# Optimization experiments

Measured on AMD Instinct MI355X. Metric: run time of the kernel, lower is better.

The kernel has to match this reference:

```python
import jax, jax.numpy as jnp
import numpy as np

B, S, T, E, H = 16, 96, 50, 128, 128
D2 = 2 * H
V = 32000
NGRAM = 2
ALPHA = 0.25


def _lstm(x, Wih, Whh, b, reverse=False):
    # x: [N, T, E] -> outputs [N, T, H], final h, c (PyTorch gate order i,f,g,o)
    xt = jnp.swapaxes(x, 0, 1)
    if reverse:
        xt = xt[::-1]
    n = x.shape[0]
    h = Whh.shape[1]
    init = (jnp.zeros((n, h), x.dtype), jnp.zeros((n, h), x.dtype))

    def step(carry, xin):
        hprev, cprev = carry
        g = xin @ Wih.T + hprev @ Whh.T + b
        i, f, gg, o = jnp.split(g, 4, axis=-1)
        c = jax.nn.sigmoid(f) * cprev + jax.nn.sigmoid(i) * jnp.tanh(gg)
        hnew = jax.nn.sigmoid(o) * jnp.tanh(c)
        return (hnew, c), hnew

    (hT, cT), outs = jax.lax.scan(step, init, xt)
    if reverse:
        outs = outs[::-1]
    return jnp.swapaxes(outs, 0, 1), hT, cT


def _gru(x, h, Wi, Wh, bi, bh):
    # PyTorch GRUCell, gate order r,z,n
    gi = x @ Wi.T + bi
    gh = h @ Wh.T + bh
    ir, iz, inn = jnp.split(gi, 3, axis=-1)
    hr, hz, hn = jnp.split(gh, 3, axis=-1)
    r = jax.nn.sigmoid(ir + hr)
    z = jax.nn.sigmoid(iz + hz)
    n = jnp.tanh(inn + r * hn)
    return (1.0 - z) * n + z * h


def _norm_scale(x):
    # (||x|| + alpha) / (||x|| + 1), detached as in the original
    v = jnp.linalg.norm(x, axis=1)
    return jax.lax.stop_gradient(((v + ALPHA) / (v + 1.0))[:, None])


def setup_inputs() -> dict:
    key = jax.random.key(0)
    ks = jax.random.split(key, 30)
    rn = lambda k, sh: jax.random.normal(k, sh, jnp.float32) * 0.05
    return {
        "enc_batch": jax.random.randint(ks[0], (B * S, T), 0, V),
        "struct_parent": jax.random.randint(ks[1], (B, S, S), 0, B * S + 1),
        "struct_child": jax.random.randint(ks[2], (B, S, S), 0, B * S + 1),
        "mask_emb": (jax.random.uniform(ks[3], (B, S, S, 1)) < 0.2).astype(jnp.float32),
        "emb_table": rn(ks[4], (V, E)),
        "Wih_f": rn(ks[5], (4 * H, E)), "Whh_f": rn(ks[6], (4 * H, H)), "b_f": rn(ks[7], (4 * H,)),
        "Wih_b": rn(ks[8], (4 * H, E)), "Whh_b": rn(ks[9], (4 * H, H)), "b_b": rn(ks[10], (4 * H,)),
        "Wc": rn(ks[11], (H, D2)), "bc": rn(ks[12], (H,)),
        "Whr": rn(ks[13], (H, D2)), "bhr": rn(ks[14], (H,)),
        "Wi_cp": rn(ks[15], (3 * D2, D2)), "Wh_cp": rn(ks[16], (3 * D2, D2)),
        "bi_cp": rn(ks[17], (3 * D2,)), "bh_cp": rn(ks[18], (3 * D2,)),
        "Wi_pc": rn(ks[19], (3 * D2, D2)), "Wh_pc": rn(ks[20], (3 * D2, D2)),
        "bi_pc": rn(ks[21], (3 * D2,)), "bh_pc": rn(ks[22], (3 * D2,)),
    }


def reference(enc_batch, struct_parent, struct_child, mask_emb, emb_table,
              Wih_f, Whh_f, b_f, Wih_b, Whh_b, b_b, Wc, bc, Whr, bhr,
              Wi_cp, Wh_cp, bi_cp, bh_cp, Wi_pc, Wh_pc, bi_pc, bh_pc):
    # Sentence encoder (bidirectional LSTM); dropout=0 -> identity
    emb = emb_table[enc_batch]                       # [B*S, T, E]
    _, hf, cf = _lstm(emb, Wih_f, Whh_f, b_f)
    _, hb, cb = _lstm(emb, Wih_b, Whh_b, b_b, reverse=True)
    c_red = jax.nn.relu(jnp.concatenate([cf, cb], 1) @ Wc.T + bc)
    h_red = jax.nn.relu(jnp.concatenate([hf, hb], 1) @ Whr.T + bhr)
    enc_states = jnp.concatenate([c_red, h_red], 1)  # [B*S, 2H]
    zero = jnp.zeros((1, D2), enc_states.dtype)
    hidden = jnp.concatenate([zero, enc_states], 0)  # [B*S+1, 2H]; row 0 = zero_emb

    # child -> parent message passing
    for _ in range(NGRAM):
        p = hidden[struct_parent].reshape(-1, D2)    # gather [B*S*S, 2H]
        c = hidden[struct_child].reshape(-1, D2)
        ch = _gru(c, p, Wi_cp, Wh_cp, bi_cp, bh_cp).reshape(B, S, S, D2)
        ch = (ch * mask_emb).sum(1).reshape(B * S, D2)
        ch = jnp.concatenate([zero, ch], 0)
        hidden = hidden + ch * _norm_scale(ch)

    # parent -> child message passing
    for _ in range(NGRAM):
        p = hidden[struct_parent].reshape(-1, D2)
        c = hidden[struct_child].reshape(-1, D2)
        ch = _gru(p, c, Wi_pc, Wh_pc, bi_pc, bh_pc).reshape(B, S, S, D2)
        ch = (ch * mask_emb).sum(2).reshape(B * S, D2)
        ch = jnp.concatenate([zero, ch], 0)
        hidden = hidden + ch * _norm_scale(ch)

    return hidden
```

## Files before the change

kernel.cpp:

```cpp
#include <hip/hip_runtime.h>

typedef unsigned short u16;
typedef __attribute__((ext_vector_type(8))) short bf8;
typedef __attribute__((ext_vector_type(4))) short s16x4;
typedef __attribute__((ext_vector_type(4))) float f32x4;
typedef __attribute__((ext_vector_type(4))) int   i32x4;
typedef __attribute__((ext_vector_type(2))) int   i32x2;

#define S_   96
#define T_   50
#define NSEQ 1536
#define NR   1537
#define XROW 520
#define L2E   1.4426950408889634f
#define L2E2  2.8853900817779268f

__device__ __forceinline__ float bf2f(u16 u){ return __uint_as_float(((unsigned)u)<<16); }
__device__ __forceinline__ u16 f2bf(float f){
  unsigned u = __float_as_uint(f);
  u += 0x7fffu + ((u>>16)&1u);
  return (u16)(u>>16);
}
__device__ __forceinline__ int cvtpk(float lo, float hi){
  int r; asm("v_cvt_pk_bf16_f32 %0, %1, %2" : "=v"(r) : "v"(lo), "v"(hi)); return r;
}
#if __has_builtin(__builtin_amdgcn_exp2f)
__device__ __forceinline__ float exp2_(float x){ return __builtin_amdgcn_exp2f(x); }
#else
__device__ __forceinline__ float exp2_(float x){ return exp2f(x); }
#endif
__device__ __forceinline__ float sigm(float x){
  return __builtin_amdgcn_rcpf(1.f + __expf(-x));
}
__device__ __forceinline__ float tanh_(float x){
  return 1.f - 2.f*__builtin_amdgcn_rcpf(__expf(2.f*x) + 1.f);
}
__device__ __forceinline__ void bar_lds(){
  asm volatile("s_waitcnt lgkmcnt(0)\n\ts_barrier" ::: "memory");
}

struct CvtArgs { const float* s[10]; u16* d[10]; };
__global__ __launch_bounds__(256) void prep_kernel(CvtArgs a,
    const int* __restrict__ par, const int* __restrict__ chi,
    const float* __restrict__ mask,
    int2* __restrict__ ent0, int* __restrict__ cnt0,
    int2* __restrict__ ent1, int* __restrict__ cnt1)
{
  if (blockIdx.x < 1088){
    int e = (blockIdx.x*256 + threadIdx.x)*4;
    if (e >= 1114112) return;
    int t, off;
    if (e < 262144){ t = e>>16; off = e & 65535; }
    else if (e < 327680){ int e2=e-262144; t = 4+(e2>>15); off = e2&32767; }
    else { int e3=e-327680; t = 6 + e3/196608; off = e3%196608; }
    int src = off;
    if (t < 4){
      int colp = off>>7, k = off&127;
      int orig = ((colp>>4)&3)*128 + ((colp>>6)<<4) + (colp&15);
      src = orig*128 + k;
    }
    f32x4 v = *reinterpret_cast<const f32x4*>(a.s[t]+src);
    i32x2 o;
    o[0] = cvtpk(v[0], v[1]);
    o[1] = cvtpk(v[2], v[3]);
    *reinterpret_cast<i32x2*>(a.d[t]+off) = o;
  } else {
    const int rr = blockIdx.x - 1088;
    __shared__ int c0s, c1s;
    if (threadIdx.x==0){ c0s=0; c1s=0; }
    __syncthreads();
    const int l = threadIdx.x;
    if (l < S_){
      const int b = rr/S_, fx = rr%S_, base = b*S_*S_;
      int idx = base + l*S_ + fx;
      if (mask[idx] != 0.f){
        int p = atomicAdd(&c0s, 1);
        ent0[rr*S_ + p] = make_int2(chi[idx], par[idx]);
      }
      int jdx = base + fx*S_ + l;
      if (mask[jdx] != 0.f){
        int p = atomicAdd(&c1s, 1);
        ent1[rr*S_ + p] = make_int2(par[jdx], chi[jdx]);
      }
    }
    __syncthreads();
    if (threadIdx.x==0){ cnt0[rr]=c0s; cnt1[rr]=c1s; }
  }
}

__global__ __launch_bounds__(512, 2) void lstm_kernel(
    const int* __restrict__ enc, const float* __restrict__ emb,
    const u16* __restrict__ WihF, const u16* __restrict__ WhhF, const float* __restrict__ bF,
    const u16* __restrict__ WihB, const u16* __restrict__ WhhB, const float* __restrict__ bB,
    u16* __restrict__ c_cat, u16* __restrict__ h_cat)
{
  __shared__ short xh[16*XROW];
  __shared__ int   toks[16*T_];

  const int tid  = threadIdx.x;
  const int wave = tid>>6;
  const int lane = tid&63;
  const int dir  = blockIdx.y;
  const int s0   = blockIdx.x*16;

  const u16* Wih = dir ? WihB : WihF;
  const u16* Whh = dir ? WhhB : WhhF;
  const float* bb = dir ? bB  : bF;

  for (int i=tid; i<16*T_; i+=512)
    toks[i] = enc[(s0 + i/T_)*T_ + (i%T_)];

  const int mL   = lane&15;
  const int quad = lane>>4;
  const int kb   = quad*8;

  bf8 Breg[4][8];
  f32x4 sbias[4];
  #pragma unroll
  for (int n=0;n<4;n++){
    int colp = wave*64 + n*16 + mL;
    f32x4 bv = *reinterpret_cast<const f32x4*>(bb + n*128 + wave*16 + quad*4);
    float sc = (n==2) ? L2E2 : -L2E;
    #pragma unroll
    for (int i=0;i<4;i++) sbias[n][i] = bv[i]*sc;
    #pragma unroll
    for (int ks=0;ks<8;ks++){
      int k = ks*32 + kb;
      const u16* p = (k<128) ? (Wih + colp*128 + k) : (Whh + colp*128 + (k-128));
      Breg[n][ks] = *reinterpret_cast<const bf8*>(p);
      asm volatile("" : "+v"(Breg[n][ks]));
    }
  }

  if (tid<256){
    int r = tid>>4, c = tid&15;
    *reinterpret_cast<i32x4*>(&xh[r*XROW + 256 + c*8]) = (i32x4){0,0,0,0};
  }

  const int srow = tid>>5, schunk = tid&31;
  float cst[4] = {0.f,0.f,0.f,0.f};
  float hst[4] = {0.f,0.f,0.f,0.f};

  __syncthreads();

  {
    int tok0 = toks[srow*T_ + (dir ? (T_-1) : 0)];
    f32x4 x0 = *reinterpret_cast<const f32x4*>(emb + tok0*128 + schunk*4);
    int tok1 = toks[srow*T_ + (dir ? (T_-2) : 1)];
    f32x4 x1 = *reinterpret_cast<const f32x4*>(emb + tok1*128 + schunk*4);
    i32x2 p0; p0[0]=cvtpk(x0[0],x0[1]); p0[1]=cvtpk(x0[2],x0[3]);
    i32x2 p1; p1[0]=cvtpk(x1[0],x1[1]); p1[1]=cvtpk(x1[2],x1[3]);
    *reinterpret_cast<i32x2*>(&xh[srow*XROW +       schunk*4]) = p0;
    *reinterpret_cast<i32x2*>(&xh[srow*XROW + 128 + schunk*4]) = p1;
  }
  f32x4 xvA, xvB;
  {
    int tA = toks[srow*T_ + (dir ? (T_-3) : 2)];
    xvA = *reinterpret_cast<const f32x4*>(emb + tA*128 + schunk*4);
    int tB = toks[srow*T_ + (dir ? (T_-4) : 3)];
    xvB = *reinterpret_cast<const f32x4*>(emb + tB*128 + schunk*4);
  }
  __syncthreads();

  f32x4 accx[4];
  #pragma unroll
  for (int n=0;n<4;n++) accx[n] = (f32x4){0.f,0.f,0.f,0.f};
  #pragma unroll
  for (int ks=0;ks<4;ks++){
    bf8 b = *reinterpret_cast<const bf8*>(&xh[mL*XROW + ks*32 + kb]);
    #pragma unroll
    for (int n=0;n<4;n++)
      accx[n] = __builtin_amdgcn_mfma_f32_16x16x32_bf16(Breg[n][ks], b, accx[n], 0,0,0);
  }
  bar_lds();

  for (int t=0;t<T_;t++){
    const int cb = t&1, nb = cb^1;

    f32x4 acc[4];
    {
      bf8 b = *reinterpret_cast<const bf8*>(&xh[mL*XROW + 256 + cb*128 + kb]);
      #pragma unroll
      for (int n=0;n<4;n++)
        acc[n] = __builtin_amdgcn_mfma_f32_16x16x32_bf16(Breg[n][4], b, accx[n], 0,0,0);
    }
    #pragma unroll
    for (int ks=1;ks<4;ks++){
      bf8 b = *reinterpret_cast<const bf8*>(&xh[mL*XROW + 256 + cb*128 + ks*32 + kb]);
      #pragma unroll
      for (int n=0;n<4;n++)
        acc[n] = __builtin_amdgcn_mfma_f32_16x16x32_bf16(Breg[n][4+ks], b, acc[n], 0,0,0);
    }

    if (t+2 < T_){
      i32x2 p; p[0]=cvtpk(xvA[0],xvA[1]); p[1]=cvtpk(xvA[2],xvA[3]);
      *reinterpret_cast<i32x2*>(&xh[srow*XROW + cb*128 + schunk*4]) = p;
    }
    xvA = xvB;
    if (t+4 < T_){
      int tok = toks[srow*T_ + (dir ? (T_-5-t) : (t+4))];
      xvB = *reinterpret_cast<const f32x4*>(emb + tok*128 + schunk*4);
    }

    if (t+1 < T_){
      #pragma unroll
      for (int n=0;n<4;n++) accx[n] = (f32x4){0.f,0.f,0.f,0.f};
      #pragma unroll
      for (int ks=0;ks<4;ks++){
        bf8 b = *reinterpret_cast<const bf8*>(&xh[mL*XROW + nb*128 + ks*32 + kb]);
        #pragma unroll
        for (int n=0;n<4;n++)
          accx[n] = __builtin_amdgcn_mfma_f32_16x16x32_bf16(Breg[n][ks], b, accx[n], 0,0,0);
      }
    }

    float hv4[4];
    #pragma unroll
    for (int i=0;i<4;i++){
      float si = __builtin_amdgcn_rcpf(1.f + exp2_(fmaf(acc[0][i], -L2E, sbias[0][i])));
      float sf = __builtin_amdgcn_rcpf(1.f + exp2_(fmaf(acc[1][i], -L2E, sbias[1][i])));
      float so = __builtin_amdgcn_rcpf(1.f + exp2_(fmaf(acc[3][i], -L2E, sbias[3][i])));
      float tg = 1.f - 2.f*__builtin_amdgcn_rcpf(exp2_(fmaf(acc[2][i], L2E2, sbias[2][i])) + 1.f);
      float c  = sf*cst[i] + si*tg;
      float th = 1.f - 2.f*__builtin_amdgcn_rcpf(exp2_(c*L2E2) + 1.f);
      float h  = so*th;
      cst[i]=c; hst[i]=h; hv4[i]=h;
    }
    if (t != T_-1){
      i32x2 hp;
      hp[0]=cvtpk(hv4[0],hv4[1]); hp[1]=cvtpk(hv4[2],hv4[3]);
      *reinterpret_cast<i32x2*>(&xh[mL*XROW + 256 + nb*128 + wave*16 + quad*4]) = hp;
      bar_lds();
    }
  }

  {
    const int ch = wave*16 + quad*4;
    const int gs = s0 + mL;
    i32x2 cp_, hp_;
    cp_[0]=cvtpk(cst[0],cst[1]); cp_[1]=cvtpk(cst[2],cst[3]);
    hp_[0]=cvtpk(hst[0],hst[1]); hp_[1]=cvtpk(hst[2],hst[3]);
    *reinterpret_cast<i32x2*>(c_cat + gs*256 + dir*128 + ch) = cp_;
    *reinterpret_cast<i32x2*>(h_cat + gs*256 + dir*128 + ch) = hp_;
  }
}

__global__ __launch_bounds__(256) void reduce_kernel(
    const u16* __restrict__ c_cat, const u16* __restrict__ h_cat,
    const u16* __restrict__ Wc, const float* __restrict__ bc,
    const u16* __restrict__ Whr, const float* __restrict__ bhr,
    float* __restrict__ hidf, u16* __restrict__ hidb)
{
  const int tid=threadIdx.x, wave=tid>>6, lane=tid&63;
  const int mL=lane&15, quad=lane>>4, kb=quad*8;
  const int m0 = blockIdx.x*16;
  const u16* A    = (wave<2) ? c_cat : h_cat;
  const u16* W    = (wave<2) ? Wc  : Whr;
  const float* bv = (wave<2) ? bc  : bhr;
  const int nb    = (wave&1)*64;
  const int obase = (wave<2) ? 0 : 128;

  f32x4 acc[4];
  #pragma unroll
  for (int nt=0;nt<4;nt++) acc[nt] = (f32x4){0.f,0.f,0.f,0.f};

  #pragma unroll
  for (int ks=0;ks<8;ks++){
    int k = ks*32 + kb;
    bf8 bfr[4];
    #pragma unroll
    for (int nt=0;nt<4;nt++)
      bfr[nt] = *reinterpret_cast<const bf8*>(W + (nb+nt*16+mL)*256 + k);
    bf8 a = *reinterpret_cast<const bf8*>(A + (m0+mL)*256 + k);
    #pragma unroll
    for (int nt=0;nt<4;nt++)
      acc[nt] = __builtin_amdgcn_mfma_f32_16x16x32_bf16(a, bfr[nt], acc[nt], 0,0,0);
  }
  const int row0 = quad*4;
  float biasv[4];
  #pragma unroll
  for (int nt=0;nt<4;nt++) biasv[nt] = bv[nb+nt*16+mL];
  #pragma unroll
  for (int nt=0;nt<4;nt++){
    int col = obase + nb + nt*16 + mL;
    #pragma unroll
    for (int i=0;i<4;i++){
      int r = m0 + row0 + i;
      float v = fmaxf(acc[nt][i] + biasv[nt], 0.f);
      hidf[(r+1)*256 + col] = v;
      hidb[(r+1)*256 + col] = f2bf(v);
    }
  }
  if (blockIdx.x==0 && tid<64){
    #pragma unroll
    for (int j=0;j<4;j++){ hidf[tid*4+j] = 0.f; hidb[tid*4+j] = 0; }
  }
}

__global__ __launch_bounds__(256) void gates_gemm_kernel(
    const u16* __restrict__ hidb,
    const u16* __restrict__ Wi, const u16* __restrict__ Wh,
    const float* __restrict__ bi, const float* __restrict__ bh,
    u16* __restrict__ gi, u16* __restrict__ gh)
{
  const int tid=threadIdx.x, wave=tid>>6, lane=tid&63;
  const int mL=lane&15, quad=lane>>4, kb=quad*8;
  const int m0 = blockIdx.x*32;
  const int n0 = blockIdx.y*128 + wave*32;
  const bool isI = (n0 < 768);
  const u16* W    = isI ? Wi : Wh;
  const float* bv = isI ? bi : bh;
  u16* out        = isI ? gi : gh;
  const int nbc   = isI ? n0 : (n0-768);

  int arow[2];
  #pragma unroll
  for (int mt=0;mt<2;mt++) arow[mt] = min(m0+mt*16+mL, NR-1);

  f32x4 acc[2][2];
  #pragma unroll
  for (int mt=0;mt<2;mt++)
    #pragma unroll
    for (int nt=0;nt<2;nt++) acc[mt][nt] = (f32x4){0.f,0.f,0.f,0.f};

  #pragma unroll
  for (int ks=0;ks<8;ks++){
    int k = ks*32 + kb;
    bf8 bfr[2];
    #pragma unroll
    for (int nt=0;nt<2;nt++)
      bfr[nt] = *reinterpret_cast<const bf8*>(W + (nbc+nt*16+mL)*256 + k);
    #pragma unroll
    for (int mt=0;mt<2;mt++){
      bf8 a = *reinterpret_cast<const bf8*>(hidb + arow[mt]*256 + k);
      #pragma unroll
      for (int nt=0;nt<2;nt++)
        acc[mt][nt] = __builtin_amdgcn_mfma_f32_16x16x32_bf16(a, bfr[nt], acc[mt][nt], 0,0,0);
    }
  }
  const int row0 = quad*4;
  float biasv[2];
  #pragma unroll
  for (int nt=0;nt<2;nt++) biasv[nt] = bv[nbc+nt*16+mL];
  #pragma unroll
  for (int mt=0;mt<2;mt++){
    #pragma unroll
    for (int nt=0;nt<2;nt++){
      #pragma unroll
      for (int i=0;i<4;i++){
        int r = m0 + mt*16 + row0 + i;
        if (r < NR)
          out[r*768 + nbc + nt*16 + mL] = f2bf(acc[mt][nt][i] + biasv[nt]);
      }
    }
  }
}

__global__ __launch_bounds__(512) void pair_kernel(
    const u16* __restrict__ gi, const u16* __restrict__ gh,
    const float* __restrict__ hin,
    float* __restrict__ hout, u16* __restrict__ bout, float* __restrict__ dout,
    const int2* __restrict__ ent, const int* __restrict__ cnt)
{
  const int r = blockIdx.x;
  const int tid = threadIdx.x, wave = tid>>6, lane = tid&63;
  __shared__ float part[8][260];
  __shared__ float ssum[4];
  if (r==0){
    if (tid<256){
      hout[tid]=0.f; bout[tid]=0;
      if (dout) dout[tid]=0.f;
    }
    return;
  }
  const int rr = r-1;
  const int n  = cnt[rr];
  const int2* e = ent + rr*S_;
  const int ch0 = lane*4;

  float a0=0.f, a1=0.f, a2=0.f, a3=0.f;
  for (int k=wave; k<n; k+=8){
    int2 pr = e[k];
    const u16* gx = gi + pr.x*768 + ch0;
    const u16* gy = gh + pr.y*768 + ch0;
    s16x4 vi0 = *reinterpret_cast<const s16x4*>(gx);
    s16x4 vi1 = *reinterpret_cast<const s16x4*>(gx+256);
    s16x4 vi2 = *reinterpret_cast<const s16x4*>(gx+512);
    s16x4 vh0 = *reinterpret_cast<const s16x4*>(gy);
    s16x4 vh1 = *reinterpret_cast<const s16x4*>(gy+256);
    s16x4 vh2 = *reinterpret_cast<const s16x4*>(gy+512);
    f32x4 hv  = *reinterpret_cast<const f32x4*>(hin + pr.y*256 + ch0);
    float o[4];
    #pragma unroll
    for (int i=0;i<4;i++){
      float rg = sigm(bf2f((u16)vi0[i]) + bf2f((u16)vh0[i]));
      float zg = sigm(bf2f((u16)vi1[i]) + bf2f((u16)vh1[i]));
      float ng = tanh_(bf2f((u16)vi2[i]) + rg*bf2f((u16)vh2[i]));
      o[i] = (1.f-zg)*ng + zg*hv[i];
    }
    a0 += o[0]; a1 += o[1]; a2 += o[2]; a3 += o[3];
  }
  *reinterpret_cast<f32x4*>(&part[wave][ch0]) = (f32x4){a0,a1,a2,a3};
  __syncthreads();

  if (tid < 256){
    float tot = part[0][tid] + part[1][tid] + part[2][tid] + part[3][tid]
              + part[4][tid] + part[5][tid] + part[6][tid] + part[7][tid];
    part[0][tid] = tot;
    float sq = tot*tot;
    #pragma unroll
    for (int off=32; off>0; off>>=1) sq += __shfl_xor(sq, off, 64);
    if (lane==0) ssum[wave] = sq;
  }
  __syncthreads();
  if (tid < 256){
    float tot = part[0][tid];
    float v  = sqrtf(ssum[0]+ssum[1]+ssum[2]+ssum[3]);
    float sc = (v + 0.25f)*__builtin_amdgcn_rcpf(v + 1.f);
    float nv = hin[r*256 + tid] + tot*sc;
    hout[r*256 + tid] = nv;
    bout[r*256 + tid] = f2bf(nv);
    if (dout) dout[r*256 + tid] = nv;
  }
}

extern "C" void kernel_launch(void* const* d_in, const int* in_sizes, int n_in,
                              void* d_out, int out_size, void* d_ws, size_t ws_size,
                              hipStream_t stream)
{
  const int*   enc  = (const int*)  d_in[0];
  const int*   spar = (const int*)  d_in[1];
  const int*   schi = (const int*)  d_in[2];
  const float* mask = (const float*)d_in[3];
  const float* emb  = (const float*)d_in[4];
  const float* WihF = (const float*)d_in[5];
  const float* WhhF = (const float*)d_in[6];
  const float* bF   = (const float*)d_in[7];
  const float* WihB = (const float*)d_in[8];
  const float* WhhB = (const float*)d_in[9];
  const float* bB   = (const float*)d_in[10];
  const float* Wc   = (const float*)d_in[11];
  const float* bc   = (const float*)d_in[12];
  const float* Whr  = (const float*)d_in[13];
  const float* bhr  = (const float*)d_in[14];
  const float* WiCP = (const float*)d_in[15];
  const float* WhCP = (const float*)d_in[16];
  const float* biCP = (const float*)d_in[17];
  const float* bhCP = (const float*)d_in[18];
  const float* WiPC = (const float*)d_in[19];
  const float* WhPC = (const float*)d_in[20];
  const float* biPC = (const float*)d_in[21];
  const float* bhPC = (const float*)d_in[22];

  char* ws = (char*)d_ws;
  u16*   c_cat = (u16*)  (ws + 0);
  u16*   h_cat = (u16*)  (ws + 786432);
  float* hf0   = (float*)(ws + 1572864);
  float* hf1   = (float*)(ws + 3146752);
  u16*   hb    = (u16*)  (ws + 4720640);
  u16*   gi    = (u16*)  (ws + 5507584);
  u16*   gh    = (u16*)  (ws + 7868416);
  u16*   wbf   = (u16*)  (ws + 10229248);
  int2*  ent0  = (int2*) (ws + 12457472);
  int2*  ent1  = (int2*) (ws + 13637120);
  int*   cnt0  = (int*)  (ws + 14816768);
  int*   cnt1  = (int*)  (ws + 14822912);
  float* out   = (float*)d_out;

  u16* bWihF = wbf + 0;
  u16* bWhhF = wbf + 65536;
  u16* bWihB = wbf + 131072;
  u16* bWhhB = wbf + 196608;
  u16* bWc   = wbf + 262144;
  u16* bWhr  = wbf + 294912;
  u16* bWiCP = wbf + 327680;
  u16* bWhCP = wbf + 524288;
  u16* bWiPC = wbf + 720896;
  u16* bWhPC = wbf + 917504;

  CvtArgs ca;
  ca.s[0]=WihF; ca.s[1]=WhhF; ca.s[2]=WihB; ca.s[3]=WhhB;
  ca.s[4]=Wc;   ca.s[5]=Whr;
  ca.s[6]=WiCP; ca.s[7]=WhCP; ca.s[8]=WiPC; ca.s[9]=WhPC;
  ca.d[0]=bWihF; ca.d[1]=bWhhF; ca.d[2]=bWihB; ca.d[3]=bWhhB;
  ca.d[4]=bWc;   ca.d[5]=bWhr;
  ca.d[6]=bWiCP; ca.d[7]=bWhCP; ca.d[8]=bWiPC; ca.d[9]=bWhPC;
  prep_kernel<<<dim3(1088+NSEQ), dim3(256), 0, stream>>>(
      ca, spar, schi, mask, ent0, cnt0, ent1, cnt1);

  lstm_kernel<<<dim3(96,2), dim3(512), 0, stream>>>(
      enc, emb, bWihF,bWhhF,bF, bWihB,bWhhB,bB, c_cat, h_cat);
  reduce_kernel<<<dim3(96), dim3(256), 0, stream>>>(
      c_cat,h_cat, bWc,bc,bWhr,bhr, hf0,hb);

  float* hfb[2] = {hf0,hf1};
  int cur = 0;
  for (int it=0; it<4; it++){
    const u16* Wi   = (it<2)?bWiCP:bWiPC;
    const u16* Wh   = (it<2)?bWhCP:bWhPC;
    const float* bi = (it<2)?biCP:biPC;
    const float* bh = (it<2)?bhCP:bhPC;
    int nxt = cur^1;
    gates_gemm_kernel<<<dim3(49,12), dim3(256), 0, stream>>>(
        hb, Wi,Wh,bi,bh, gi,gh);
    pair_kernel<<<dim3(NR), dim3(512), 0, stream>>>(
        gi,gh, hfb[cur], hfb[nxt], hb,
        (it==3)?out:(float*)nullptr,
        (it<2)?ent0:ent1, (it<2)?cnt0:cnt1);
    cur = nxt;
  }
}
```

Baseline: 306.9 us.

## Merge prep into LSTM launch and fuse reduce with first gates GEMM

The weight-conversion/entry-building prep kernel is merged into the LSTM kernel as extra blocks, so the LSTM reads fp32 weights directly and converts them to bf16 in registers, dropping a launch and one dependency. The reduce GEMM is fused into the first GRU gates GEMM: each block recomputes its 32 hidden rows into LDS and consumes them immediately, removing another launch. The cost is that reduce work is recomputed across the 12 column blocks, and the LSTM blocks now load fp32 weights with the permutation applied on the fly.

```diff
diff --git a/kernel.cpp b/kernel.cpp
--- a/kernel.cpp
+++ b/kernel.cpp
@@ -40,72 +40,68 @@
 }
 
 struct CvtArgs { const float* s[10]; u16* d[10]; };
-__global__ __launch_bounds__(256) void prep_kernel(CvtArgs a,
+
+__global__ __launch_bounds__(512, 2) void mega_kernel(
+    const int* __restrict__ enc, const float* __restrict__ emb,
+    const float* __restrict__ WihF, const float* __restrict__ WhhF, const float* __restrict__ bF,
+    const float* __restrict__ WihB, const float* __restrict__ WhhB, const float* __restrict__ bB,
+    u16* __restrict__ c_cat, u16* __restrict__ h_cat,
+    CvtArgs ca,
     const int* __restrict__ par, const int* __restrict__ chi,
     const float* __restrict__ mask,
     int2* __restrict__ ent0, int* __restrict__ cnt0,
     int2* __restrict__ ent1, int* __restrict__ cnt1)
 {
-  if (blockIdx.x < 1088){
-    int e = (blockIdx.x*256 + threadIdx.x)*4;
-    if (e >= 1114112) return;
-    int t, off;
-    if (e < 262144){ t = e>>16; off = e & 65535; }
-    else if (e < 327680){ int e2=e-262144; t = 4+(e2>>15); off = e2&32767; }
-    else { int e3=e-327680; t = 6 + e3/196608; off = e3%196608; }
-    int src = off;
-    if (t < 4){
-      int colp = off>>7, k = off&127;
-      int orig = ((colp>>4)&3)*128 + ((colp>>6)<<4) + (colp&15);
-      src = orig*128 + k;
-    }
-    f32x4 v = *reinterpret_cast<const f32x4*>(a.s[t]+src);
-    i32x2 o;
-    o[0] = cvtpk(v[0], v[1]);
-    o[1] = cvtpk(v[2], v[3]);
-    *reinterpret_cast<i32x2*>(a.d[t]+off) = o;
-  } else {
-    const int rr = blockIdx.x - 1088;
-    __shared__ int c0s, c1s;
-    if (threadIdx.x==0){ c0s=0; c1s=0; }
-    __syncthreads();
-    const int l = threadIdx.x;
-    if (l < S_){
-      const int b = rr/S_, fx = rr%S_, base = b*S_*S_;
-      int idx = base + l*S_ + fx;
-      if (mask[idx] != 0.f){
-        int p = atomicAdd(&c0s, 1);
-        ent0[rr*S_ + p] = make_int2(chi[idx], par[idx]);
-      }
-      int jdx = base + fx*S_ + l;
-      if (mask[jdx] != 0.f){
-        int p = atomicAdd(&c1s, 1);
-        ent1[rr*S_ + p] = make_int2(par[jdx], chi[jdx]);
-      }
-    }
-    __syncthreads();
-    if (threadIdx.x==0){ cnt0[rr]=c0s; cnt1[rr]=c1s; }
-  }
-}
-
-__global__ __launch_bounds__(512, 2) void lstm_kernel(
-    const int* __restrict__ enc, const float* __restrict__ emb,
-    const u16* __restrict__ WihF, const u16* __restrict__ WhhF, const float* __restrict__ bF,
-    const u16* __restrict__ WihB, const u16* __restrict__ WhhB, const float* __restrict__ bB,
-    u16* __restrict__ c_cat, u16* __restrict__ h_cat)
-{
   __shared__ short xh[16*XROW];
   __shared__ int   toks[16*T_];
-
-  const int tid  = threadIdx.x;
+  __shared__ int   c0s, c1s;
+
+  const int bid = blockIdx.x;
+  const int tid = threadIdx.x;
+
+  if (bid >= 192){
+    if (bid < 608){
+      int e = 262144 + ((bid-192)*512 + tid)*4;
+      int t, off;
+      if (e < 327680){ int e2=e-262144; t = 4+(e2>>15); off = e2&32767; }
+      else { int e3=e-327680; t = 6 + e3/196608; off = e3%196608; }
+      f32x4 v = *reinterpret_cast<const f32x4*>(ca.s[t]+off);
+      i32x2 o;
+      o[0] = cvtpk(v[0], v[1]);
+      o[1] = cvtpk(v[2], v[3]);
+      *reinterpret_cast<i32x2*>(ca.d[t]+off) = o;
+    } else {
+      const int rr = bid - 608;
+      if (tid==0){ c0s=0; c1s=0; }
+      __syncthreads();
+      const int l = tid;
+      if (l < S_){
+        const int b = rr/S_, fx = rr%S_, base = b*S_*S_;
+        int idx = base + l*S_ + fx;
+        if (mask[idx] != 0.f){
+          int p = atomicAdd(&c0s, 1);
+          ent0[rr*S_ + p] = make_int2(chi[idx], par[idx]);
+        }
+        int jdx = base + fx*S_ + l;
+        if (mask[jdx] != 0.f){
+          int p = atomicAdd(&c1s, 1);
+          ent1[rr*S_ + p] = make_int2(par[jdx], chi[jdx]);
+        }
+      }
+      __syncthreads();
+      if (tid==0){ cnt0[rr]=c0s; cnt1[rr]=c1s; }
+    }
+    return;
+  }
+
   const int wave = tid>>6;
   const int lane = tid&63;
-  const int dir  = blockIdx.y;
-  const int s0   = blockIdx.x*16;
-
-  const u16* Wih = dir ? WihB : WihF;
-  const u16* Whh = dir ? WhhB : WhhF;
-  const float* bb = dir ? bB  : bF;
+  const int dir  = bid/96;
+  const int s0   = (bid%96)*16;
+
+  const float* Wih = dir ? WihB : WihF;
+  const float* Whh = dir ? WhhB : WhhF;
+  const float* bb  = dir ? bB  : bF;
 
   for (int i=tid; i<16*T_; i+=512)
     toks[i] = enc[(s0 + i/T_)*T_ + (i%T_)];
@@ -119,6 +115,7 @@
   #pragma unroll
   for (int n=0;n<4;n++){
     int colp = wave*64 + n*16 + mL;
+    int orig = ((colp>>4)&3)*128 + ((colp>>6)<<4) + (colp&15);
     f32x4 bv = *reinterpret_cast<const f32x4*>(bb + n*128 + wave*16 + quad*4);
     float sc = (n==2) ? L2E2 : -L2E;
     #pragma unroll
@@ -126,8 +123,13 @@
     #pragma unroll
     for (int ks=0;ks<8;ks++){
       int k = ks*32 + kb;
-      const u16* p = (k<128) ? (Wih + colp*128 + k) : (Whh + colp*128 + (k-128));
-      Breg[n][ks] = *reinterpret_cast<const bf8*>(p);
+      const float* pf = (k<128) ? (Wih + orig*128 + k) : (Whh + orig*128 + (k-128));
+      f32x4 w0 = *reinterpret_cast<const f32x4*>(pf);
+      f32x4 w1 = *reinterpret_cast<const f32x4*>(pf+4);
+      i32x4 q;
+      q[0]=cvtpk(w0[0],w0[1]); q[1]=cvtpk(w0[2],w0[3]);
+      q[2]=cvtpk(w1[0],w1[1]); q[3]=cvtpk(w1[2],w1[3]);
+      Breg[n][ks] = *reinterpret_cast<bf8*>(&q);
       asm volatile("" : "+v"(Breg[n][ks]));
     }
   }
@@ -245,55 +247,121 @@
   }
 }
 
-__global__ __launch_bounds__(256) void reduce_kernel(
+__global__ __launch_bounds__(256) void rgates_kernel(
     const u16* __restrict__ c_cat, const u16* __restrict__ h_cat,
-    const u16* __restrict__ Wc, const float* __restrict__ bc,
+    const u16* __restrict__ Wc,  const float* __restrict__ bc,
     const u16* __restrict__ Whr, const float* __restrict__ bhr,
-    float* __restrict__ hidf, u16* __restrict__ hidb)
+    float* __restrict__ hidf, u16* __restrict__ hidb,
+    const u16* __restrict__ Wi, const u16* __restrict__ Wh,
+    const float* __restrict__ bi, const float* __restrict__ bh,
+    u16* __restrict__ gi, u16* __restrict__ gh)
 {
+  __shared__ u16 hl[32][264];
+
   const int tid=threadIdx.x, wave=tid>>6, lane=tid&63;
   const int mL=lane&15, quad=lane>>4, kb=quad*8;
-  const int m0 = blockIdx.x*16;
-  const u16* A    = (wave<2) ? c_cat : h_cat;
-  const u16* W    = (wave<2) ? Wc  : Whr;
-  const float* bv = (wave<2) ? bc  : bhr;
-  const int nb    = (wave&1)*64;
-  const int obase = (wave<2) ? 0 : 128;
-
-  f32x4 acc[4];
-  #pragma unroll
-  for (int nt=0;nt<4;nt++) acc[nt] = (f32x4){0.f,0.f,0.f,0.f};
+  const int g0 = blockIdx.x*32;
+
+  {
+    const u16* A    = (wave<2) ? c_cat : h_cat;
+    const u16* W    = (wave<2) ? Wc  : Whr;
+    const float* bv = (wave<2) ? bc  : bhr;
+    const int nb_   = (wave&1)*64;
+    const int obase = (wave<2) ? 0 : 128;
+
+    #pragma unroll
+    for (int p=0;p<2;p++){
+      const int base = g0 + p*16 - 1;
+      f32x4 acc[4];
+      #pragma unroll
+      for (int nt=0;nt<4;nt++) acc[nt] = (f32x4){0.f,0.f,0.f,0.f};
+
+      int ar = base + mL;
+      ar = (ar < 0) ? 0 : ((ar > 1535) ? 1535 : ar);
+
+      #pragma unroll
+      for (int ks=0;ks<8;ks++){
+        int k = ks*32 + kb;
+        bf8 bfr[4];
+        #pragma unroll
+        for (int nt=0;nt<4;nt++)
+          bfr[nt] = *reinterpret_cast<const bf8*>(W + (nb_+nt*16+mL)*256 + k);
+        bf8 a = *reinterpret_cast<const bf8*>(A + ar*256 + k);
+        #pragma unroll
+        for (int nt=0;nt<4;nt++)
+          acc[nt] = __builtin_amdgcn_mfma_f32_16x16x32_bf16(a, bfr[nt], acc[nt], 0,0,0);
+      }
+      float biasv[4];
+      #pragma unroll
+      for (int nt=0;nt<4;nt++) biasv[nt] = bv[nb_+nt*16+mL];
+      #pragma unroll
+      for (int nt=0;nt<4;nt++){
+        int col = obase + nb_ + nt*16 + mL;
+        #pragma unroll
+        for (int i=0;i<4;i++){
+          int g = base + quad*4 + i + 1;
+          float v = fmaxf(acc[nt][i] + biasv[nt], 0.f);
+          if (g == 0) v = 0.f;
+          u16 hv16 = f2bf(v);
+          hl[g - g0][col] = hv16;
+          if (g <= 1536){
+            hidf[g*256 + col] = v;
+            hidb[g*256 + col] = hv16;
+          }
+        }
+      }
+    }
+  }
+  __syncthreads();
+
+  const int m0 = g0;
+  const int n0 = blockIdx.y*128 + wave*32;
+  const bool isI = (n0 < 768);
+  const u16* W    = isI ? Wi : Wh;
+  const float* bv = isI ? bi : bh;
+  u16* out        = isI ? gi : gh;
+  const int nbc   = isI ? n0 : (n0-768);
+
+  int aslot[2];
+  #pragma unroll
+  for (int mt=0;mt<2;mt++) aslot[mt] = min(m0+mt*16+mL, NR-1) - g0;
+
+  f32x4 acc[2][2];
+  #pragma unroll
+  for (int mt=0;mt<2;mt++)
+    #pragma unroll
+    for (int nt=0;nt<2;nt++) acc[mt][nt] = (f32x4){0.f,0.f,0.f,0.f};
 
   #pragma unroll
   for (int ks=0;ks<8;ks++){
     int k = ks*32 + kb;
-    bf8 bfr[4];
-    #pragma unroll
-    for (int nt=0;nt<4;nt++)
-      bfr[nt] = *reinterpret_cast<const bf8*>(W + (nb+nt*16+mL)*256 + k);
-    bf8 a = *reinterpret_cast<const bf8*>(A + (m0+mL)*256 + k);
-    #pragma unroll
-    for (int nt=0;nt<4;nt++)
-      acc[nt] = __builtin_amdgcn_mfma_f32_16x16x32_bf16(a, bfr[nt], acc[nt], 0,0,0);
+    bf8 bfr[2];
+    #pragma unroll
+    for (int nt=0;nt<2;nt++)
+      bfr[nt] = *reinterpret_cast<const bf8*>(W + (nbc+nt*16+mL)*256 + k);
+    #pragma unroll
+    for (int mt=0;mt<2;mt++){
+      bf8 a = *reinterpret_cast<const bf8*>(&hl[aslot[mt]][k]);
+      #pragma unroll
+      for (int nt=0;nt<2;nt++)
+        acc[mt][nt] = __builtin_amdgcn_mfma_f32_16x16x32_bf16(a, bfr[nt], acc[mt][nt], 0,0,0);
+    }
   }
   const int row0 = quad*4;
-  float biasv[4];
-  #pragma unroll
-  for (int nt=0;nt<4;nt++) biasv[nt] = bv[nb+nt*16+mL];
-  #pragma unroll
-  for (int nt=0;nt<4;nt++){
-    int col = obase + nb + nt*16 + mL;
-    #pragma unroll
-    for (int i=0;i<4;i++){
-      int r = m0 + row0 + i;
-      float v = fmaxf(acc[nt][i] + biasv[nt], 0.f);
-      hidf[(r+1)*256 + col] = v;
-      hidb[(r+1)*256 + col] = f2bf(v);
-    }
-  }
-  if (blockIdx.x==0 && tid<64){
-    #pragma unroll
-    for (int j=0;j<4;j++){ hidf[tid*4+j] = 0.f; hidb[tid*4+j] = 0; }
+  float biasv[2];
+  #pragma unroll
+  for (int nt=0;nt<2;nt++) biasv[nt] = bv[nbc+nt*16+mL];
+  #pragma unroll
+  for (int mt=0;mt<2;mt++){
+    #pragma unroll
+    for (int nt=0;nt<2;nt++){
+      #pragma unroll
+      for (int i=0;i<4;i++){
+        int r = m0 + mt*16 + row0 + i;
+        if (r < NR)
+          out[r*768 + nbc + nt*16 + mL] = f2bf(acc[mt][nt][i] + biasv[nt]);
+      }
+    }
   }
 }
 
@@ -467,10 +535,6 @@
   int*   cnt1  = (int*)  (ws + 14822912);
   float* out   = (float*)d_out;
 
-  u16* bWihF = wbf + 0;
-  u16* bWhhF = wbf + 65536;
-  u16* bWihB = wbf + 131072;
-  u16* bWhhB = wbf + 196608;
   u16* bWc   = wbf + 262144;
   u16* bWhr  = wbf + 294912;
   u16* bWiCP = wbf + 327680;
@@ -482,27 +546,30 @@
   ca.s[0]=WihF; ca.s[1]=WhhF; ca.s[2]=WihB; ca.s[3]=WhhB;
   ca.s[4]=Wc;   ca.s[5]=Whr;
   ca.s[6]=WiCP; ca.s[7]=WhCP; ca.s[8]=WiPC; ca.s[9]=WhPC;
-  ca.d[0]=bWihF; ca.d[1]=bWhhF; ca.d[2]=bWihB; ca.d[3]=bWhhB;
+  ca.d[0]=wbf;        ca.d[1]=wbf+65536;  ca.d[2]=wbf+131072; ca.d[3]=wbf+196608;
   ca.d[4]=bWc;   ca.d[5]=bWhr;
   ca.d[6]=bWiCP; ca.d[7]=bWhCP; ca.d[8]=bWiPC; ca.d[9]=bWhPC;
-  prep_kernel<<<dim3(1088+NSEQ), dim3(256), 0, stream>>>(
+
+  mega_kernel<<<dim3(192+416+1536), dim3(512), 0, stream>>>(
+      enc, emb, WihF, WhhF, bF, WihB, WhhB, bB, c_cat, h_cat,
       ca, spar, schi, mask, ent0, cnt0, ent1, cnt1);
 
-  lstm_kernel<<<dim3(96,2), dim3(512), 0, stream>>>(
-      enc, emb, bWihF,bWhhF,bF, bWihB,bWhhB,bB, c_cat, h_cat);
-  reduce_kernel<<<dim3(96), dim3(256), 0, stream>>>(
-      c_cat,h_cat, bWc,bc,bWhr,bhr, hf0,hb);
+  rgates_kernel<<<dim3(49,12), dim3(256), 0, stream>>>(
+      c_cat, h_cat, bWc, bc, bWhr, bhr, hf0, hb,
+      bWiCP, bWhCP, biCP, bhCP, gi, gh);
 
   float* hfb[2] = {hf0,hf1};
   int cur = 0;
   for (int it=0; it<4; it++){
-    const u16* Wi   = (it<2)?bWiCP:bWiPC;
-    const u16* Wh   = (it<2)?bWhCP:bWhPC;
-    const float* bi = (it<2)?biCP:biPC;
-    const float* bh = (it<2)?bhCP:bhPC;
+    if (it > 0){
+      const u16* Wi   = (it<2)?bWiCP:bWiPC;
+      const u16* Wh   = (it<2)?bWhCP:bWhPC;
+      const float* bi = (it<2)?biCP:biPC;
+      const float* bh = (it<2)?bhCP:bhPC;
+      gates_gemm_kernel<<<dim3(49,12), dim3(256), 0, stream>>>(
+          hb, Wi,Wh,bi,bh, gi,gh);
+    }
     int nxt = cur^1;
-    gates_gemm_kernel<<<dim3(49,12), dim3(256), 0, stream>>>(
-        hb, Wi,Wh,bi,bh, gi,gh);
     pair_kernel<<<dim3(NR), dim3(512), 0, stream>>>(
         gi,gh, hfb[cur], hfb[nxt], hb,
         (it==3)?out:(float*)nullptr,
```

New measurement: 319.4 us. +4.1%, slower.
